# Kernel optimization log

Hardware: AMD Instinct MI355X
Metric: run time of the kernel (lower is better)

The kernel has to match this reference:

```python
import jax, jax.numpy as jnp
import numpy as np

V, E, H, TAG, B, S = 100000, 128, 256, 16, 64, 512
T = TAG + 2            # tag_size + start + end
START, END = T - 2, T - 1


def setup_inputs() -> dict:
    key = jax.random.key(0)
    ks = jax.random.split(key, 16)
    x = jax.random.randint(ks[0], (B, S), 0, V)
    lengths = jax.random.randint(ks[1], (B,), S // 2, S + 1)
    mask = (jnp.arange(S)[None, :] < lengths[:, None]).astype(jnp.int32)

    def rn(k, shape, s=0.05):
        return (jax.random.normal(k, shape) * s).astype(jnp.float32)

    embed = rn(ks[2], (V, E), 0.1)
    Wih_f = rn(ks[3], (4 * H, E)); Whh_f = rn(ks[4], (4 * H, H))
    bih_f = rn(ks[5], (4 * H,));   bhh_f = rn(ks[6], (4 * H,))
    Wih_b = rn(ks[7], (4 * H, E)); Whh_b = rn(ks[8], (4 * H, H))
    bih_b = rn(ks[9], (4 * H,));   bhh_b = rn(ks[10], (4 * H,))
    Wc = rn(ks[11], (T, 2 * H));   bc = rn(ks[12], (T,))
    trans = rn(ks[13], (T, T), 0.1)
    trans = trans.at[:, START].set(-1000.0).at[END, :].set(-1000.0)
    h0 = rn(ks[14], (2, B, H), 1.0)  # init_hidden uses randn
    c0 = rn(ks[15], (2, B, H), 1.0)
    return dict(x=x, mask=mask, embed=embed,
                Wih_f=Wih_f, Whh_f=Whh_f, bih_f=bih_f, bhh_f=bhh_f,
                Wih_b=Wih_b, Whh_b=Whh_b, bih_b=bih_b, bhh_b=bhh_b,
                Wc=Wc, bc=bc, trans=trans, h0=h0, c0=c0)


def _lstm_dir(xs, h0, c0, Wih, Whh, bih, bhh, reverse):
    # xs: [S,B,E]; PyTorch gate order i,f,g,o
    xp = jnp.einsum('sbe,ge->sbg', xs, Wih) + bih  # batch the input GEMM

    def step(carry, xg):
        h, c = carry
        g = xg + h @ Whh.T + bhh
        i, f, gg, o = jnp.split(g, 4, axis=-1)
        c = jax.nn.sigmoid(f) * c + jax.nn.sigmoid(i) * jnp.tanh(gg)
        h = jax.nn.sigmoid(o) * jnp.tanh(c)
        return (h, c), h

    _, hs = jax.lax.scan(step, (h0, c0), xp, reverse=reverse)
    return hs  # [S,B,H]


def _viterbi(feats, mask, trans):
    # feats [B,S,T]; scores[t,b,prev,cur] = feats[t,b,cur] + trans[prev,cur]
    scores = feats.transpose(1, 0, 2)[:, :, None, :] + trans[None, None, :, :]  # [S,B,T,T]
    mT = mask.T  # [S,B]
    partition0 = scores[0, :, START, :]  # [B,T]

    def step(partition, inp):
        sc_t, m_t = inp
        cur = sc_t + partition[:, :, None]        # add over prev-tag axis
        new_p = jnp.max(cur, axis=1)
        bp = jnp.argmax(cur, axis=1).astype(jnp.int32)
        bp = jnp.where(m_t[:, None] > 0, bp, 0)   # zero back-pointers at pad
        return new_p, (new_p, bp)

    _, (parts, bps) = jax.lax.scan(step, partition0, (scores[1:], mT[1:]))
    part_hist = jnp.concatenate([partition0[None], parts], axis=0)  # [S,B,T]

    lengths = jnp.sum(mask, axis=1)
    last_pos = lengths - 1  # [B]
    ph_b = part_hist.transpose(1, 0, 2)  # [B,S,T]
    last_part = jnp.take_along_axis(ph_b, last_pos[:, None, None], axis=1)[:, 0, :]  # [B,T]
    last_vals = last_part[:, :, None] + trans[None]
    max_value = jnp.max(last_vals, axis=1)                    # [B,T]
    last_bp = jnp.argmax(last_vals, axis=1).astype(jnp.int32)
    pointer = last_bp[:, END]                                  # [B]

    back = jnp.concatenate([bps, jnp.zeros((1, B, T), jnp.int32)], axis=0)  # [S,B,T]
    bp_b = back.transpose(1, 0, 2)  # [B,S,T]
    bp_b = bp_b.at[jnp.arange(B), last_pos].set(pointer[:, None])  # insert_last scatter
    back = bp_b.transpose(1, 0, 2)

    def trace(ptr, bp_t):
        new = jnp.take_along_axis(bp_t, ptr[:, None], axis=1)[:, 0]
        return new, new

    _, dec = jax.lax.scan(trace, pointer, back[:-1], reverse=True)  # [S-1,B]
    decode = jnp.concatenate([dec, pointer[None]], axis=0).T        # [B,S]
    path_score = max_value[:, END]
    return path_score, decode


def reference(x, mask, embed, Wih_f, Whh_f, bih_f, bhh_f,
              Wih_b, Whh_b, bih_b, bhh_b, Wc, bc, trans, h0, c0):
    xs = embed[x].transpose(1, 0, 2)  # [S,B,E]
    hf = _lstm_dir(xs, h0[0], c0[0], Wih_f, Whh_f, bih_f, bhh_f, False)
    hb = _lstm_dir(xs, h0[1], c0[1], Wih_b, Whh_b, bih_b, bhh_b, True)
    out = jnp.concatenate([hf, hb], axis=-1)            # [S,B,2H]
    feats = (out @ Wc.T + bc).transpose(1, 0, 2)        # [B,S,T]
    return _viterbi(feats, mask, trans)
```

## Files before the change

kernel.cpp:

```cpp
#include <hip/hip_runtime.h>

#define SLEN 512
#define BATCH 64
#define HID 256
#define EMB 128
#define NT 18
#define BQ 2
#define NGROUP 64
#define NFLAG 8
#define FB 8
#define SB 4

typedef unsigned int u32;

__device__ __forceinline__ float sigmoidf_(float v) { return 1.0f / (1.0f + expf(-v)); }
__device__ __forceinline__ u32 aload(const u32* p) {
  return __hip_atomic_load((u32*)p, __ATOMIC_RELAXED, __HIP_MEMORY_SCOPE_AGENT);
}

__global__ __launch_bounds__(512, 2) void lstm_kernel(
    const int* __restrict__ x, const float* __restrict__ embed,
    const float* __restrict__ Wih_f, const float* __restrict__ Whh_f,
    const float* __restrict__ bih_f, const float* __restrict__ bhh_f,
    const float* __restrict__ Wih_b, const float* __restrict__ Whh_b,
    const float* __restrict__ bih_b, const float* __restrict__ bhh_b,
    const float* __restrict__ h0, const float* __restrict__ c0,
    float* __restrict__ h_hist, u32* __restrict__ flags)
{
  const int g    = blockIdx.x & 63;
  const int rk   = blockIdx.x >> 6;
  const int dir  = g >> 5;
  const int b0   = (g & 31) * BQ;
  const int tid  = threadIdx.x;
  const int row  = tid & 255;
  const int kh   = tid >> 8;
  const int gi   = row >> 6;
  const int uo   = row & 63;
  const int grow = gi * 256 + rk * 64 + uo;
  const int wv   = tid >> 6;
  const int lane = tid & 63;

  const float* Wih = dir ? Wih_b : Wih_f;
  const float* Whh = dir ? Whh_b : Whh_f;
  const float* bih = dir ? bih_b : bih_f;
  const float* bhh = dir ? bhh_b : bhh_f;

  float4 wreg[48];
  if (kh == 0) {
#pragma unroll
    for (int c = 0; c < 48; ++c)
      wreg[c] = *(const float4*)(Whh + (size_t)grow * 256 + c * 4);
  } else {
#pragma unroll
    for (int c = 0; c < 16; ++c)
      wreg[c] = *(const float4*)(Whh + (size_t)grow * 256 + 192 + c * 4);
#pragma unroll
    for (int c = 0; c < 32; ++c)
      wreg[16 + c] = *(const float4*)(Wih + (size_t)grow * 128 + c * 4);
  }
  const int vb = kh ? 192 : 0;

  __shared__ float vlds[BQ][384];
  __shared__ float red[2][2][BQ][256];

  const bool isgate = (wv >= 6);
  float bias4[4] = {0, 0, 0, 0};
  float creg = 0.0f;
  int gb = 0;
  if (isgate) {
    gb = (tid - 384) >> 6;
#pragma unroll
    for (int gg = 0; gg < 4; ++gg) {
      int rr = gg * 256 + rk * 64 + lane;
      bias4[gg] = bih[rr] + bhh[rr];
    }
    creg = c0[(size_t)(dir * BATCH + b0 + gb) * HID + rk * 64 + lane];
  }

  const int eb = tid >> 7, ee = tid & 127;
  float ev = 0.0f; int xv = 0;
  if (tid < 256) {
    ev = embed[(size_t)x[(b0 + eb) * SLEN + (dir ? SLEN - 1 : 0)] * EMB + ee];
    xv = x[(b0 + eb) * SLEN + (dir ? SLEN - 2 : 1)];
  }

  for (int it = 0; it < SLEN; ++it) {
    const int t = dir ? (SLEN - 1 - it) : it;

    if (!isgate) {
      if (tid < 256) vlds[eb][256 + ee] = ev;
      if (it == 0) {
        const float* hs = h0 + (size_t)(dir * BATCH + b0) * HID;
        vlds[tid >> 8][tid & 255] = hs[tid];
        if (tid < 128) vlds[1][tid + 128] = hs[tid + 384];
      } else {
        const u32* fp = flags + ((size_t)g * SLEN + (it - 1)) * NFLAG + (lane & 7);
        u32 v = aload(fp);
        int sp = 0;
        while (!__all(v != 0) && ++sp < (1 << 14)) {
          __builtin_amdgcn_s_sleep(1);
          v = aload(fp);
        }
        asm volatile("" ::: "memory");
        const int tp = dir ? (t + 1) : (t - 1);
        const u32* hs = (const u32*)(h_hist +
                         ((size_t)(dir * SLEN + tp) * BATCH + b0) * HID);
        u32 a0 = aload(hs + tid);
        u32 a1 = (tid < 128) ? aload(hs + tid + 384) : 0u;
        *(u32*)&vlds[tid >> 8][tid & 255] = a0;
        if (tid < 128) *(u32*)&vlds[1][tid + 128] = a1;
      }
    }
    __syncthreads();

    if (tid < 256) {
      ev = embed[(size_t)xv * EMB + ee];
      int sn = it + 2 < SLEN ? it + 2 : SLEN - 1;
      xv = x[(b0 + eb) * SLEN + (dir ? (SLEN - 1 - sn) : sn)];
    }

    float a0 = 0.0f, a1 = 0.0f;
#pragma unroll
    for (int c = 0; c < 48; ++c) {
      float4 w4 = wreg[c];
      float4 v0 = *(const float4*)&vlds[0][vb + c * 4];
      float4 v1 = *(const float4*)&vlds[1][vb + c * 4];
      a0 = fmaf(w4.x, v0.x, a0); a0 = fmaf(w4.y, v0.y, a0);
      a0 = fmaf(w4.z, v0.z, a0); a0 = fmaf(w4.w, v0.w, a0);
      a1 = fmaf(w4.x, v1.x, a1); a1 = fmaf(w4.y, v1.y, a1);
      a1 = fmaf(w4.z, v1.z, a1); a1 = fmaf(w4.w, v1.w, a1);
    }
    red[it & 1][kh][0][row] = a0;
    red[it & 1][kh][1][row] = a1;
    __syncthreads();

    if (isgate) {
      const int p = it & 1;
      float s0 = bias4[0] + red[p][0][gb][lane]       + red[p][1][gb][lane];
      float s1 = bias4[1] + red[p][0][gb][64 + lane]  + red[p][1][gb][64 + lane];
      float s2 = bias4[2] + red[p][0][gb][128 + lane] + red[p][1][gb][128 + lane];
      float s3 = bias4[3] + red[p][0][gb][192 + lane] + red[p][1][gb][192 + lane];
      float ig = sigmoidf_(s0);
      float fg = sigmoidf_(s1);
      float gv = tanhf(s2);
      float og = sigmoidf_(s3);
      creg = fg * creg + ig * gv;
      float hv = og * tanhf(creg);
      __hip_atomic_store(h_hist + ((size_t)(dir * SLEN + t) * BATCH + (b0 + gb)) * HID
                           + rk * 64 + lane,
                         hv, __ATOMIC_RELAXED, __HIP_MEMORY_SCOPE_AGENT);
      asm volatile("s_waitcnt vmcnt(0)" ::: "memory");
      if (lane == 0)
        __hip_atomic_store(flags + ((size_t)g * SLEN + it) * NFLAG + rk * 2 + (wv - 6),
                           1u, __ATOMIC_RELAXED, __HIP_MEMORY_SCOPE_AGENT);
    }
  }
}

__global__ __launch_bounds__(256) void feats_kernel(
    const float* __restrict__ h_hist, const float* __restrict__ Wc,
    const float* __restrict__ bc, float* __restrict__ feats)
{
  const int s0  = (blockIdx.x >> 3) * SB;
  const int b0  = (blockIdx.x & 7) * FB;
  const int tid = threadIdx.x;
  __shared__ float wc[NT * 516];
  __shared__ float hl[FB * 516];
  __shared__ float bcl[NT];
  if (tid < NT) bcl[tid] = bc[tid];
  for (int f = tid * 4; f < NT * 512; f += 1024) {
    float4 v = *(const float4*)(Wc + f);
    *(float4*)&wc[(f >> 9) * 516 + (f & 511)] = v;
  }
  for (int si = 0; si < SB; ++si) {
    const int s = s0 + si;
    const float* src0 = h_hist + ((size_t)s * BATCH + b0) * HID;
    const float* src1 = h_hist + ((size_t)(SLEN + s) * BATCH + b0) * HID;
    for (int f = tid * 4; f < FB * 256; f += 1024) {
      int b = f >> 8, j = f & 255;
      *(float4*)&hl[b * 516 + j]       = *(const float4*)(src0 + f);
      *(float4*)&hl[b * 516 + 256 + j] = *(const float4*)(src1 + f);
    }
    __syncthreads();
    if (tid < FB * NT) {
      int b = tid / NT, tag = tid - b * NT;
      float a = bcl[tag];
      const float* hp = &hl[b * 516];
      const float* wp = &wc[tag * 516];
#pragma unroll 8
      for (int k = 0; k < 512; k += 4) {
        float4 h4 = *(const float4*)(hp + k);
        float4 w4 = *(const float4*)(wp + k);
        a = fmaf(h4.x, w4.x, a); a = fmaf(h4.y, w4.y, a);
        a = fmaf(h4.z, w4.z, a); a = fmaf(h4.w, w4.w, a);
      }
      feats[((size_t)s * BATCH + b0 + b) * NT + tag] = a;
    }
    __syncthreads();
  }
}

__global__ __launch_bounds__(64) void viterbi_kernel(
    const float* __restrict__ feats, const int* __restrict__ mask,
    const float* __restrict__ trans, float* __restrict__ out)
{
  const int b = blockIdx.x;
  const int lane = threadIdx.x;
  __shared__ float tr[NT][NT + 1];
  __shared__ float part[2][NT + 2];
  __shared__ float lastp[NT + 2];
  __shared__ unsigned char bp[SLEN][20];
  __shared__ int len_s;

  for (int f = lane; f < NT * NT; f += 64) tr[f / NT][f % NT] = trans[f];
  int m = 0;
#pragma unroll
  for (int i = 0; i < 8; ++i) m += mask[b * SLEN + lane * 8 + i];
  for (int off = 32; off; off >>= 1) m += __shfl_down(m, off);
  if (lane == 0) len_s = m;
  __syncthreads();
  const int len = len_s;

  if (lane < NT) part[0][lane] = feats[(size_t)b * NT + lane] + tr[16][lane];
  __syncthreads();

  int cur = 0;
  float fnext = (lane < NT) ? feats[((size_t)BATCH + b) * NT + lane] : 0.0f;
  int   mnext = mask[b * SLEN + 1];
  for (int t = 1; t < SLEN; ++t) {
    float fcur = fnext; int mcur = mnext;
    if (t < SLEN - 1) {
      fnext = (lane < NT) ? feats[((size_t)(t + 1) * BATCH + b) * NT + lane] : 0.0f;
      mnext = mask[b * SLEN + t + 1];
    }
    if (lane < NT) {
      float best = -3.0e38f; int bf = 0;
#pragma unroll
      for (int from = 0; from < NT; ++from) {
        float v = (fcur + tr[from][lane]) + part[cur][from];
        if (v > best) { best = v; bf = from; }
      }
      part[cur ^ 1][lane] = best;
      bp[t][lane] = mcur ? (unsigned char)bf : (unsigned char)0;
      if (t == len - 1) lastp[lane] = best;
    }
    cur ^= 1;
    __syncthreads();
  }

  if (lane == 0) {
    float best = -3.0e38f; int bf = 0;
    for (int from = 0; from < NT; ++from) {
      float v = lastp[from] + tr[from][17];
      if (v > best) { best = v; bf = from; }
    }
    out[b] = best;
    int ptr = bf;
    out[BATCH + (size_t)b * SLEN + (SLEN - 1)] = (float)ptr;
    for (int i = SLEN - 2; i >= 0; --i) {
      int nw = (i == len - 1) ? bf : (int)bp[i + 1][ptr];
      out[BATCH + (size_t)b * SLEN + i] = (float)nw;
      ptr = nw;
    }
  }
}

extern "C" void kernel_launch(void* const* d_in, const int* in_sizes, int n_in,
                              void* d_out, int out_size, void* d_ws, size_t ws_size,
                              hipStream_t stream) {
  const int*   x      = (const int*)  d_in[0];
  const int*   mask   = (const int*)  d_in[1];
  const float* embed  = (const float*)d_in[2];
  const float* Wih_f  = (const float*)d_in[3];
  const float* Whh_f  = (const float*)d_in[4];
  const float* bih_f  = (const float*)d_in[5];
  const float* bhh_f  = (const float*)d_in[6];
  const float* Wih_b  = (const float*)d_in[7];
  const float* Whh_b  = (const float*)d_in[8];
  const float* bih_b  = (const float*)d_in[9];
  const float* bhh_b  = (const float*)d_in[10];
  const float* Wc     = (const float*)d_in[11];
  const float* bc     = (const float*)d_in[12];
  const float* trans  = (const float*)d_in[13];
  const float* h0     = (const float*)d_in[14];
  const float* c0     = (const float*)d_in[15];
  float* out = (float*)d_out;

  char* ws = (char*)d_ws;
  float* h_hist = (float*)ws;
  u32*   flags  = (u32*)(ws + (size_t)67108864);
  float* feats  = (float*)(ws + (size_t)67108864);

  hipMemsetAsync(flags, 0, (size_t)NGROUP * SLEN * NFLAG * sizeof(u32), stream);
  lstm_kernel<<<256, 512, 0, stream>>>(x, embed, Wih_f, Whh_f, bih_f, bhh_f,
                                       Wih_b, Whh_b, bih_b, bhh_b, h0, c0,
                                       h_hist, flags);
  feats_kernel<<<(SLEN / SB) * 8, 256, 0, stream>>>(h_hist, Wc, bc, feats);
  viterbi_kernel<<<BATCH, 64, 0, stream>>>(feats, mask, trans, out);
}
```

Baseline: 2.157 ms.

## Ping-pong two independent batch chains per block to hide cross-block sync latency

Each block previously handled two batch rows in lockstep: it waited on flags for both, then ran one fused matvec. It now treats the two rows as independent recurrence chains with per-chain flags and alternates half-steps, so chain B's flag wait and h reload overlap chain A's matvec and gate work, and the reverse. The aim is to hide the inter-block flag-polling and global h-reload latency on the serial critical path. The cost is four barriers per step instead of two, and weight registers are no longer shared across both rows within one FMA loop.

```diff
diff --git a/kernel.cpp b/kernel.cpp
--- a/kernel.cpp
+++ b/kernel.cpp
@@ -5,9 +5,7 @@
 #define HID 256
 #define EMB 128
 #define NT 18
-#define BQ 2
-#define NGROUP 64
-#define NFLAG 8
+#define NCHAIN 128
 #define FB 8
 #define SB 4
 
@@ -27,10 +25,11 @@
     const float* __restrict__ h0, const float* __restrict__ c0,
     float* __restrict__ h_hist, u32* __restrict__ flags)
 {
-  const int g    = blockIdx.x & 63;
   const int rk   = blockIdx.x >> 6;
-  const int dir  = g >> 5;
-  const int b0   = (g & 31) * BQ;
+  const int q    = blockIdx.x & 63;
+  const int dir  = q >> 5;
+  const int bA   = (q & 31) * 2, bB = bA + 1;
+  const int chA  = dir * BATCH + bA, chB = chA + 1;
   const int tid  = threadIdx.x;
   const int row  = tid & 255;
   const int kh   = tid >> 8;
@@ -60,100 +59,142 @@
   }
   const int vb = kh ? 192 : 0;
 
-  __shared__ float vlds[BQ][384];
-  __shared__ float red[2][2][BQ][256];
-
-  const bool isgate = (wv >= 6);
+  __shared__ float vA[384], vB[384];
+  __shared__ float redA[2][256], redB[2][256];
+
   float bias4[4] = {0, 0, 0, 0};
   float creg = 0.0f;
-  int gb = 0;
-  if (isgate) {
-    gb = (tid - 384) >> 6;
+  if (wv >= 6) {
+    int b = (wv == 6) ? bA : bB;
 #pragma unroll
     for (int gg = 0; gg < 4; ++gg) {
       int rr = gg * 256 + rk * 64 + lane;
       bias4[gg] = bih[rr] + bhh[rr];
     }
-    creg = c0[(size_t)(dir * BATCH + b0 + gb) * HID + rk * 64 + lane];
-  }
-
-  const int eb = tid >> 7, ee = tid & 127;
-  float ev = 0.0f; int xv = 0;
+    creg = c0[(size_t)(dir * BATCH + b) * HID + rk * 64 + lane];
+  }
+
+  auto TS = [&](int s) { s = s < SLEN ? s : SLEN - 1; return dir ? (SLEN - 1 - s) : s; };
+
+  const int ee = tid - 256;
+  float evA = 0.0f, evB = 0.0f;
+  int xvA = 0, xvB = 0;
+
   if (tid < 256) {
-    ev = embed[(size_t)x[(b0 + eb) * SLEN + (dir ? SLEN - 1 : 0)] * EMB + ee];
-    xv = x[(b0 + eb) * SLEN + (dir ? SLEN - 2 : 1)];
-  }
+    vA[tid] = h0[(size_t)(dir * BATCH + bA) * HID + tid];
+    vB[tid] = h0[(size_t)(dir * BATCH + bB) * HID + tid];
+  } else if (tid < 384) {
+    vA[256 + ee] = embed[(size_t)x[bA * SLEN + TS(0)] * EMB + ee];
+    evA = embed[(size_t)x[bA * SLEN + TS(1)] * EMB + ee];
+    xvA = x[bA * SLEN + TS(2)];
+    evB = embed[(size_t)x[bB * SLEN + TS(0)] * EMB + ee];
+    xvB = x[bB * SLEN + TS(1)];
+  }
+  __syncthreads();
 
   for (int it = 0; it < SLEN; ++it) {
     const int t = dir ? (SLEN - 1 - it) : it;
 
-    if (!isgate) {
-      if (tid < 256) vlds[eb][256 + ee] = ev;
-      if (it == 0) {
-        const float* hs = h0 + (size_t)(dir * BATCH + b0) * HID;
-        vlds[tid >> 8][tid & 255] = hs[tid];
-        if (tid < 128) vlds[1][tid + 128] = hs[tid + 384];
-      } else {
-        const u32* fp = flags + ((size_t)g * SLEN + (it - 1)) * NFLAG + (lane & 7);
-        u32 v = aload(fp);
-        int sp = 0;
+    {
+      float acc = 0.0f;
+#pragma unroll
+      for (int c = 0; c < 48; ++c) {
+        float4 w4 = wreg[c];
+        float4 v4 = *(const float4*)&vA[vb + c * 4];
+        acc = fmaf(w4.x, v4.x, acc); acc = fmaf(w4.y, v4.y, acc);
+        acc = fmaf(w4.z, v4.z, acc); acc = fmaf(w4.w, v4.w, acc);
+      }
+      redA[kh][row] = acc;
+    }
+    __syncthreads();
+
+    if (wv == 6) {
+      float s0 = bias4[0] + redA[0][lane]       + redA[1][lane];
+      float s1 = bias4[1] + redA[0][64 + lane]  + redA[1][64 + lane];
+      float s2 = bias4[2] + redA[0][128 + lane] + redA[1][128 + lane];
+      float s3 = bias4[3] + redA[0][192 + lane] + redA[1][192 + lane];
+      float ig = sigmoidf_(s0), fg = sigmoidf_(s1);
+      float gv = tanhf(s2),     og = sigmoidf_(s3);
+      creg = fg * creg + ig * gv;
+      float hv = og * tanhf(creg);
+      __hip_atomic_store(h_hist + ((size_t)(dir * SLEN + t) * BATCH + bA) * HID
+                           + rk * 64 + lane,
+                         hv, __ATOMIC_RELAXED, __HIP_MEMORY_SCOPE_AGENT);
+      asm volatile("s_waitcnt vmcnt(0)" ::: "memory");
+      if (lane == 0)
+        __hip_atomic_store(flags + ((size_t)chA * SLEN + it) * 4 + rk, 1u,
+                           __ATOMIC_RELAXED, __HIP_MEMORY_SCOPE_AGENT);
+    } else if (wv < 4) {
+      if (it > 0) {
+        const u32* fp = flags + ((size_t)chB * SLEN + (it - 1)) * 4 + wv;
+        u32 v = aload(fp); int sp = 0;
         while (!__all(v != 0) && ++sp < (1 << 14)) {
           __builtin_amdgcn_s_sleep(1);
           v = aload(fp);
         }
         asm volatile("" ::: "memory");
         const int tp = dir ? (t + 1) : (t - 1);
-        const u32* hs = (const u32*)(h_hist +
-                         ((size_t)(dir * SLEN + tp) * BATCH + b0) * HID);
-        u32 a0 = aload(hs + tid);
-        u32 a1 = (tid < 128) ? aload(hs + tid + 384) : 0u;
-        *(u32*)&vlds[tid >> 8][tid & 255] = a0;
-        if (tid < 128) *(u32*)&vlds[1][tid + 128] = a1;
-      }
-    }
-    __syncthreads();
-
-    if (tid < 256) {
-      ev = embed[(size_t)xv * EMB + ee];
-      int sn = it + 2 < SLEN ? it + 2 : SLEN - 1;
-      xv = x[(b0 + eb) * SLEN + (dir ? (SLEN - 1 - sn) : sn)];
-    }
-
-    float a0 = 0.0f, a1 = 0.0f;
-#pragma unroll
-    for (int c = 0; c < 48; ++c) {
-      float4 w4 = wreg[c];
-      float4 v0 = *(const float4*)&vlds[0][vb + c * 4];
-      float4 v1 = *(const float4*)&vlds[1][vb + c * 4];
-      a0 = fmaf(w4.x, v0.x, a0); a0 = fmaf(w4.y, v0.y, a0);
-      a0 = fmaf(w4.z, v0.z, a0); a0 = fmaf(w4.w, v0.w, a0);
-      a1 = fmaf(w4.x, v1.x, a1); a1 = fmaf(w4.y, v1.y, a1);
-      a1 = fmaf(w4.z, v1.z, a1); a1 = fmaf(w4.w, v1.w, a1);
-    }
-    red[it & 1][kh][0][row] = a0;
-    red[it & 1][kh][1][row] = a1;
-    __syncthreads();
-
-    if (isgate) {
-      const int p = it & 1;
-      float s0 = bias4[0] + red[p][0][gb][lane]       + red[p][1][gb][lane];
-      float s1 = bias4[1] + red[p][0][gb][64 + lane]  + red[p][1][gb][64 + lane];
-      float s2 = bias4[2] + red[p][0][gb][128 + lane] + red[p][1][gb][128 + lane];
-      float s3 = bias4[3] + red[p][0][gb][192 + lane] + red[p][1][gb][192 + lane];
-      float ig = sigmoidf_(s0);
-      float fg = sigmoidf_(s1);
-      float gv = tanhf(s2);
-      float og = sigmoidf_(s3);
+        u32 hw = aload((const u32*)(h_hist +
+                    ((size_t)(dir * SLEN + tp) * BATCH + bB) * HID) + tid);
+        *(u32*)&vB[tid] = hw;
+      }
+    } else if (wv < 6) {
+      vB[256 + ee] = evB;
+      evB = embed[(size_t)xvB * EMB + ee];
+      xvB = x[bB * SLEN + TS(it + 2)];
+    }
+    __syncthreads();
+
+    {
+      float acc = 0.0f;
+#pragma unroll
+      for (int c = 0; c < 48; ++c) {
+        float4 w4 = wreg[c];
+        float4 v4 = *(const float4*)&vB[vb + c * 4];
+        acc = fmaf(w4.x, v4.x, acc); acc = fmaf(w4.y, v4.y, acc);
+        acc = fmaf(w4.z, v4.z, acc); acc = fmaf(w4.w, v4.w, acc);
+      }
+      redB[kh][row] = acc;
+    }
+    __syncthreads();
+
+    if (wv == 7) {
+      float s0 = bias4[0] + redB[0][lane]       + redB[1][lane];
+      float s1 = bias4[1] + redB[0][64 + lane]  + redB[1][64 + lane];
+      float s2 = bias4[2] + redB[0][128 + lane] + redB[1][128 + lane];
+      float s3 = bias4[3] + redB[0][192 + lane] + redB[1][192 + lane];
+      float ig = sigmoidf_(s0), fg = sigmoidf_(s1);
+      float gv = tanhf(s2),     og = sigmoidf_(s3);
       creg = fg * creg + ig * gv;
       float hv = og * tanhf(creg);
-      __hip_atomic_store(h_hist + ((size_t)(dir * SLEN + t) * BATCH + (b0 + gb)) * HID
+      __hip_atomic_store(h_hist + ((size_t)(dir * SLEN + t) * BATCH + bB) * HID
                            + rk * 64 + lane,
                          hv, __ATOMIC_RELAXED, __HIP_MEMORY_SCOPE_AGENT);
       asm volatile("s_waitcnt vmcnt(0)" ::: "memory");
       if (lane == 0)
-        __hip_atomic_store(flags + ((size_t)g * SLEN + it) * NFLAG + rk * 2 + (wv - 6),
-                           1u, __ATOMIC_RELAXED, __HIP_MEMORY_SCOPE_AGENT);
-    }
+        __hip_atomic_store(flags + ((size_t)chB * SLEN + it) * 4 + rk, 1u,
+                           __ATOMIC_RELAXED, __HIP_MEMORY_SCOPE_AGENT);
+    } else if (wv < 4) {
+      if (it < SLEN - 1) {
+        const u32* fp = flags + ((size_t)chA * SLEN + it) * 4 + wv;
+        u32 v = aload(fp); int sp = 0;
+        while (!__all(v != 0) && ++sp < (1 << 14)) {
+          __builtin_amdgcn_s_sleep(1);
+          v = aload(fp);
+        }
+        asm volatile("" ::: "memory");
+        u32 hw = aload((const u32*)(h_hist +
+                    ((size_t)(dir * SLEN + t) * BATCH + bA) * HID) + tid);
+        *(u32*)&vA[tid] = hw;
+      }
+    } else if (wv < 6) {
+      if (it < SLEN - 1) {
+        vA[256 + ee] = evA;
+        evA = embed[(size_t)xvA * EMB + ee];
+        xvA = x[bA * SLEN + TS(it + 3)];
+      }
+    }
+    __syncthreads();
   }
 }
 
@@ -291,7 +332,7 @@
   u32*   flags  = (u32*)(ws + (size_t)67108864);
   float* feats  = (float*)(ws + (size_t)67108864);
 
-  hipMemsetAsync(flags, 0, (size_t)NGROUP * SLEN * NFLAG * sizeof(u32), stream);
+  hipMemsetAsync(flags, 0, (size_t)NCHAIN * SLEN * 4 * sizeof(u32), stream);
   lstm_kernel<<<256, 512, 0, stream>>>(x, embed, Wih_f, Whh_f, bih_f, bhh_f,
                                        Wih_b, Whh_b, bih_b, bhh_b, h0, c0,
                                        h_hist, flags);
```

New measurement: 2.072 ms. -4.0%, faster.
